# Kernel optimization log

Measured on AMD Instinct MI355X. Metric: run time of the kernel, lower is better.

Reference implementation:

```python
import jax, jax.numpy as jnp
import numpy as np

N, E, B = 50000, 400000, 128
F_IN, EDIM, EMB, H = 64, 8, 64, 4
HC = EMB * H  # 256
L = 3          # gnn_layers
DN = 256       # dense_neurons
NEG_SLOPE = 0.2
EPS = 1e-5


def setup_inputs():
    key = jax.random.key(0)
    ks = jax.random.split(key, 32)
    s = 0.05
    d = {}
    d["x"] = jax.random.normal(ks[0], (N, F_IN), jnp.float32)
    d["edge_index"] = jax.random.randint(ks[1], (2, E), 0, N, jnp.int32)
    d["edge_attr"] = jax.random.normal(ks[2], (E, EDIM), jnp.float32)
    d["mol_formal_charge"] = jax.random.normal(ks[3], (B,), jnp.float32)
    d["mol_nrot"] = jax.random.normal(ks[4], (B,), jnp.float32)
    d["batch_index"] = jnp.sort(jax.random.randint(ks[5], (N,), 0, B, jnp.int32))
    # GATv2 params, stacked over L layers (in_dim == EMB == F_IN for all layers)
    d["gat_Wl"] = jax.random.normal(ks[6], (L, F_IN, HC), jnp.float32) * s
    d["gat_Wr"] = jax.random.normal(ks[7], (L, F_IN, HC), jnp.float32) * s
    d["gat_We"] = jax.random.normal(ks[8], (L, EDIM, HC), jnp.float32) * s
    d["gat_att"] = jax.random.normal(ks[9], (L, H, EMB), jnp.float32) * s
    d["gat_b"] = jnp.zeros((L, HC), jnp.float32)
    d["tr_W"] = jax.random.normal(ks[10], (L, HC, EMB), jnp.float32) * s
    d["tr_b"] = jnp.zeros((L, EMB), jnp.float32)
    d["bn_g"] = jnp.ones((L, EMB), jnp.float32)
    d["bn_b"] = jnp.zeros((L, EMB), jnp.float32)
    d["gate_W"] = jax.random.normal(ks[11], (EMB, 1), jnp.float32) * s
    d["gate_b"] = jnp.zeros((1,), jnp.float32)
    d["lin1_W"] = jax.random.normal(ks[12], (EMB + 2, DN), jnp.float32) * s
    d["lin1_b"] = jnp.zeros((DN,), jnp.float32)
    d["fc1_W"] = jax.random.normal(ks[13], (DN, DN // 2), jnp.float32) * s
    d["fc1_b"] = jnp.zeros((DN // 2,), jnp.float32)
    d["fc2_W"] = jax.random.normal(ks[14], (DN // 2, DN // 4), jnp.float32) * s
    d["fc2_b"] = jnp.zeros((DN // 4,), jnp.float32)
    d["out_W"] = jax.random.normal(ks[15], (DN // 4, 1), jnp.float32) * s
    d["out_b"] = jnp.zeros((1,), jnp.float32)
    return d


def _seg_softmax(logits, seg, num):
    # numerically stable per-segment softmax over leading axis
    mx = jax.ops.segment_max(logits, seg, num_segments=num)
    ex = jnp.exp(logits - mx[seg])
    den = jax.ops.segment_sum(ex, seg, num_segments=num)
    return ex / den[seg]


def reference(x, edge_index, edge_attr, mol_formal_charge, mol_nrot, batch_index,
              gat_Wl, gat_Wr, gat_We, gat_att, gat_b, tr_W, tr_b, bn_g, bn_b,
              gate_W, gate_b, lin1_W, lin1_b, fc1_W, fc1_b, fc2_W, fc2_b,
              out_W, out_b):
    src, dst = edge_index[0], edge_index[1]  # messages flow src -> dst
    h = x
    for l in range(L):
        xl = (h @ gat_Wl[l]).reshape(N, H, EMB)
        xr = (h @ gat_Wr[l]).reshape(N, H, EMB)
        ea = (edge_attr @ gat_We[l]).reshape(E, H, EMB)
        xls = xl[src]                                   # [E,H,C]
        m = jax.nn.leaky_relu(xls + xr[dst] + ea, NEG_SLOPE)
        logit = jnp.einsum('ehc,hc->eh', m, gat_att[l])  # [E,H]
        alpha = _seg_softmax(logit, dst, N)              # [E,H]
        agg = jax.ops.segment_sum(alpha[:, :, None] * xls, dst, num_segments=N)
        h = agg.reshape(N, HC) + gat_b[l]
        h = jax.nn.relu(h @ tr_W[l] + tr_b[l])
        # BatchNorm1d (training-mode batch stats, biased var)
        mu = h.mean(0)
        var = h.var(0)
        h = (h - mu) / jnp.sqrt(var + EPS) * bn_g[l] + bn_b[l]
    # AttentionalAggregation pooling
    gate = h @ gate_W + gate_b                           # [N,1]
    w = _seg_softmax(gate, batch_index, B)
    pooled = jax.ops.segment_sum(w * h, batch_index, num_segments=B)  # [B,EMB]
    z = jnp.concatenate([pooled, mol_formal_charge[:, None], mol_nrot[:, None]], axis=1)
    z = jax.nn.relu(z @ lin1_W + lin1_b)
    z = jax.nn.relu(z @ fc1_W + fc1_b)
    z = jax.nn.relu(z @ fc2_W + fc2_b)
    return z @ out_W + out_b                             # [B,1]
```

## Files before the change

kernel.cpp:

```cpp
#include <hip/hip_runtime.h>

#define NN 50000
#define NE 400000
#define NB 128
#define NINF (-__builtin_inff())

__device__ __forceinline__ float dpp_add16(float x) {
    int v = __float_as_int(x);
    x += __int_as_float(__builtin_amdgcn_update_dpp(0, v, 0xB1, 0xF, 0xF, true));
    v = __float_as_int(x);
    x += __int_as_float(__builtin_amdgcn_update_dpp(0, v, 0x4E, 0xF, 0xF, true));
    v = __float_as_int(x);
    x += __int_as_float(__builtin_amdgcn_update_dpp(0, v, 0x141, 0xF, 0xF, true));
    v = __float_as_int(x);
    x += __int_as_float(__builtin_amdgcn_update_dpp(0, v, 0x140, 0xF, 0xF, true));
    return x;
}

__global__ __launch_bounds__(256) void k_hist(const int* __restrict__ dstv, int* __restrict__ deg) {
    int e = blockIdx.x * 256 + threadIdx.x;
    if (e < NE) atomicAdd(&deg[dstv[e]], 1);
}

__global__ __launch_bounds__(256) void k_scan1(const int* __restrict__ deg, int* __restrict__ bsum,
                                               int* __restrict__ cnt) {
    __shared__ int ws[4];
    const int tid = threadIdx.x, lane = tid & 63, w = tid >> 6;
    const int i = blockIdx.x * 256 + tid;
    if (i < NN) cnt[i] = 0;
    int v = (i < NN) ? deg[i] : 0;
    #pragma unroll
    for (int off = 32; off; off >>= 1) v += __shfl_xor(v, off);
    if (lane == 0) ws[w] = v;
    __syncthreads();
    if (tid == 0) bsum[blockIdx.x] = ws[0] + ws[1] + ws[2] + ws[3];
}

__global__ __launch_bounds__(256) void k_scan2(const int* __restrict__ bsum, int* __restrict__ boff, int nblk,
                                               float* __restrict__ stats) {
    __shared__ int ws[4];
    const int tid = threadIdx.x, lane = tid & 63, w = tid >> 6;
    for (int i = tid; i < 2304; i += 256) stats[i] = 0.f;
    int v = (tid < nblk) ? bsum[tid] : 0;
    int incl = v;
    #pragma unroll
    for (int off = 1; off < 64; off <<= 1) {
        int t = __shfl_up(incl, off);
        if (lane >= off) incl += t;
    }
    if (lane == 63) ws[w] = incl;
    __syncthreads();
    int add = 0;
    for (int k = 0; k < w; ++k) add += ws[k];
    if (tid < nblk) boff[tid] = add + incl - v;
}

__global__ __launch_bounds__(256) void k_scan3(const int* __restrict__ deg, const int* __restrict__ boff,
                                               int* __restrict__ rowptr) {
    __shared__ int ws[4];
    const int tid = threadIdx.x, lane = tid & 63, w = tid >> 6;
    const int i = blockIdx.x * 256 + tid;
    int v = (i < NN) ? deg[i] : 0;
    int incl = v;
    #pragma unroll
    for (int off = 1; off < 64; off <<= 1) {
        int t = __shfl_up(incl, off);
        if (lane >= off) incl += t;
    }
    if (lane == 63) ws[w] = incl;
    __syncthreads();
    int add = boff[blockIdx.x];
    for (int k = 0; k < w; ++k) add += ws[k];
    if (i < NN) rowptr[i + 1] = add + incl;
    if (i == 0) rowptr[0] = 0;
}

__global__ __launch_bounds__(256) void k_scatter(const int* __restrict__ dstv, const int* __restrict__ srcv,
                                                 const float* __restrict__ eattr, const int* __restrict__ rowptr,
                                                 int* __restrict__ cnt, int* __restrict__ eid,
                                                 int* __restrict__ src_perm, float4* __restrict__ ea_perm,
                                                 int use_perm) {
    int e = blockIdx.x * 256 + threadIdx.x;
    if (e < NE) {
        int d = dstv[e];
        int pos = rowptr[d] + atomicAdd(&cnt[d], 1);
        eid[pos] = e;
        if (use_perm) {
            src_perm[pos] = srcv[e];
            ea_perm[(size_t)pos * 2] = ((const float4*)eattr)[e * 2];
            ea_perm[(size_t)pos * 2 + 1] = ((const float4*)eattr)[e * 2 + 1];
        }
    }
}

__global__ __launch_bounds__(256) void k_bnfin(float* __restrict__ st, const float* __restrict__ g,
                                               const float* __restrict__ b, const float* __restrict__ Wln,
                                               const float* __restrict__ Wrn) {
    __shared__ float sh_s[64];
    const int tid = threadIdx.x;
    if (tid < 64) {
        const float mu = st[tid] * (1.0f / (float)NN);
        const float var = st[64 + tid] * (1.0f / (float)NN) - mu * mu;
        const float rstd = rsqrtf(var + 1e-5f);
        const float sc = g[tid] * rstd;
        const float sh = fmaf(-mu, sc, b[tid]);
        st[128 + tid] = sc;
        st[192 + tid] = sh;
        sh_s[tid] = sh;
    }
    __syncthreads();
    float al = 0.f, ar = 0.f;
    for (int k = 0; k < 64; ++k) {
        al = fmaf(sh_s[k], Wln[k * 256 + tid], al);
        ar = fmaf(sh_s[k], Wrn[k * 256 + tid], ar);
    }
    st[256 + tid] = al;
    st[512 + tid] = ar;
}

__global__ __launch_bounds__(256, 4) void k_gemm64(const float* __restrict__ A, const float* __restrict__ Wl,
                                                   const float* __restrict__ Wr, float* __restrict__ Cl,
                                                   float* __restrict__ Cr, const float* __restrict__ stats) {
    __shared__ float At[16 * 132];
    __shared__ float Ws[16 * 128];
    const int tid = threadIdx.x;
    const int mat = blockIdx.y >> 1, ch = blockIdx.y & 1;
    const float* W = mat ? Wr : Wl;
    float* C = mat ? Cr : Cl;
    const int r0b = blockIdx.x * 128;
    const int cg = tid & 15;
    const int rg = tid >> 4;

    float acc[8][8];
    if (stats) {
        const float* shW = stats + 256 + mat * 256 + ch * 128;
        const float4 i0 = *(const float4*)(shW + cg * 4);
        const float4 i1 = *(const float4*)(shW + 64 + cg * 4);
        #pragma unroll
        for (int rr = 0; rr < 8; ++rr) {
            acc[rr][0] = i0.x; acc[rr][1] = i0.y; acc[rr][2] = i0.z; acc[rr][3] = i0.w;
            acc[rr][4] = i1.x; acc[rr][5] = i1.y; acc[rr][6] = i1.z; acc[rr][7] = i1.w;
        }
    } else {
        #pragma unroll
        for (int rr = 0; rr < 8; ++rr)
            #pragma unroll
            for (int j = 0; j < 8; ++j) acc[rr][j] = 0.f;
    }

    for (int kc = 0; kc < 4; ++kc) {
        if (kc) __syncthreads();
        for (int i = tid; i < 512; i += 256) {
            const int k = i >> 5, c4 = i & 31;
            float4 v = ((const float4*)W)[(kc * 16 + k) * 64 + ch * 32 + c4];
            if (stats) {
                const float s = stats[128 + kc * 16 + k];
                v.x *= s; v.y *= s; v.z *= s; v.w *= s;
            }
            ((float4*)Ws)[i] = v;
        }
        for (int i = tid; i < 512; i += 256) {
            const int r = i >> 2, c4 = i & 3;
            const int rgl = (r0b + r < NN) ? (r0b + r) : (NN - 1);
            const float4 v = ((const float4*)A)[rgl * 16 + kc * 4 + c4];
            At[(c4 * 4 + 0) * 132 + r] = v.x;
            At[(c4 * 4 + 1) * 132 + r] = v.y;
            At[(c4 * 4 + 2) * 132 + r] = v.z;
            At[(c4 * 4 + 3) * 132 + r] = v.w;
        }
        __syncthreads();
        #pragma unroll 4
        for (int k = 0; k < 16; ++k) {
            const float4 a0 = *(const float4*)(At + k * 132 + rg * 8);
            const float4 a1 = *(const float4*)(At + k * 132 + rg * 8 + 4);
            const float4 w0 = *(const float4*)(Ws + k * 128 + cg * 4);
            const float4 w1 = *(const float4*)(Ws + k * 128 + 64 + cg * 4);
            const float ar[8] = {a0.x, a0.y, a0.z, a0.w, a1.x, a1.y, a1.z, a1.w};
            #pragma unroll
            for (int rr = 0; rr < 8; ++rr) {
                acc[rr][0] = fmaf(ar[rr], w0.x, acc[rr][0]);
                acc[rr][1] = fmaf(ar[rr], w0.y, acc[rr][1]);
                acc[rr][2] = fmaf(ar[rr], w0.z, acc[rr][2]);
                acc[rr][3] = fmaf(ar[rr], w0.w, acc[rr][3]);
                acc[rr][4] = fmaf(ar[rr], w1.x, acc[rr][4]);
                acc[rr][5] = fmaf(ar[rr], w1.y, acc[rr][5]);
                acc[rr][6] = fmaf(ar[rr], w1.z, acc[rr][6]);
                acc[rr][7] = fmaf(ar[rr], w1.w, acc[rr][7]);
            }
        }
    }
    #pragma unroll
    for (int rr = 0; rr < 8; ++rr) {
        const int r = r0b + rg * 8 + rr;
        if (r < NN) {
            float* cp = C + (size_t)r * 256 + ch * 128 + cg * 4;
            *(float4*)cp = make_float4(acc[rr][0], acc[rr][1], acc[rr][2], acc[rr][3]);
            *(float4*)(cp + 64) = make_float4(acc[rr][4], acc[rr][5], acc[rr][6], acc[rr][7]);
        }
    }
}

template <bool PERM>
__global__ __launch_bounds__(256, 4) void k_agg(const float* __restrict__ xl, float* __restrict__ xragg,
                                                const float* __restrict__ att, const float* __restrict__ gatb,
                                                const int* __restrict__ rowptr, const int* __restrict__ eid,
                                                const int* __restrict__ srcv, const float* __restrict__ eattr,
                                                const int* __restrict__ src_perm, const float4* __restrict__ ea_perm,
                                                const float* __restrict__ We) {
    const int lane = threadIdx.x & 63;
    const float4 we0 = ((const float4*)(We + 0 * 256))[lane];
    const float4 we1 = ((const float4*)(We + 1 * 256))[lane];
    const float4 we2 = ((const float4*)(We + 2 * 256))[lane];
    const float4 we3 = ((const float4*)(We + 3 * 256))[lane];
    const float4 we4 = ((const float4*)(We + 4 * 256))[lane];
    const float4 we5 = ((const float4*)(We + 5 * 256))[lane];
    const float4 we6 = ((const float4*)(We + 6 * 256))[lane];
    const float4 we7 = ((const float4*)(We + 7 * 256))[lane];
    const float4 attf = ((const float4*)att)[lane];
    const float4 gbf = ((const float4*)gatb)[lane];
    const int nw = gridDim.x * (blockDim.x >> 6);
    const int wid = blockIdx.x * (blockDim.x >> 6) + (threadIdx.x >> 6);

#define LOADE(X, idx)                                                          \
    {                                                                          \
        int s_;                                                                \
        const float4* eap_;                                                    \
        if (PERM) {                                                            \
            s_ = src_perm[idx];                                                \
            eap_ = ea_perm + (size_t)(idx) * 2;                                \
        } else {                                                               \
            const int e_ = eid[idx];                                           \
            s_ = srcv[e_];                                                     \
            eap_ = (const float4*)(eattr + (size_t)e_ * 8);                    \
        }                                                                      \
        X##x = ((const float4*)(xl + (size_t)s_ * 256))[lane];                 \
        X##a = eap_[0];                                                        \
        X##b = eap_[1];                                                        \
    }

#define PROC(X)                                                                \
    {                                                                          \
        float v0 = fmaf(X##a.x, we0.x, xr.x), v1 = fmaf(X##a.x, we0.y, xr.y);  \
        float v2 = fmaf(X##a.x, we0.z, xr.z), v3 = fmaf(X##a.x, we0.w, xr.w);  \
        v0 = fmaf(X##a.y, we1.x, v0); v1 = fmaf(X##a.y, we1.y, v1);            \
        v2 = fmaf(X##a.y, we1.z, v2); v3 = fmaf(X##a.y, we1.w, v3);            \
        v0 = fmaf(X##a.z, we2.x, v0); v1 = fmaf(X##a.z, we2.y, v1);            \
        v2 = fmaf(X##a.z, we2.z, v2); v3 = fmaf(X##a.z, we2.w, v3);            \
        v0 = fmaf(X##a.w, we3.x, v0); v1 = fmaf(X##a.w, we3.y, v1);            \
        v2 = fmaf(X##a.w, we3.z, v2); v3 = fmaf(X##a.w, we3.w, v3);            \
        v0 = fmaf(X##b.x, we4.x, v0); v1 = fmaf(X##b.x, we4.y, v1);            \
        v2 = fmaf(X##b.x, we4.z, v2); v3 = fmaf(X##b.x, we4.w, v3);            \
        v0 = fmaf(X##b.y, we5.x, v0); v1 = fmaf(X##b.y, we5.y, v1);            \
        v2 = fmaf(X##b.y, we5.z, v2); v3 = fmaf(X##b.y, we5.w, v3);            \
        v0 = fmaf(X##b.z, we6.x, v0); v1 = fmaf(X##b.z, we6.y, v1);            \
        v2 = fmaf(X##b.z, we6.z, v2); v3 = fmaf(X##b.z, we6.w, v3);            \
        v0 = fmaf(X##b.w, we7.x, v0); v1 = fmaf(X##b.w, we7.y, v1);            \
        v2 = fmaf(X##b.w, we7.z, v2); v3 = fmaf(X##b.w, we7.w, v3);            \
        v0 += X##x.x; v1 += X##x.y; v2 += X##x.z; v3 += X##x.w;                \
        v0 = fmaxf(v0, 0.2f * v0); v1 = fmaxf(v1, 0.2f * v1);                  \
        v2 = fmaxf(v2, 0.2f * v2); v3 = fmaxf(v3, 0.2f * v3);                  \
        float part = v0 * attf.x;                                              \
        part = fmaf(v1, attf.y, part);                                         \
        part = fmaf(v2, attf.z, part);                                         \
        part = fmaf(v3, attf.w, part);                                         \
        part = dpp_add16(part);                                                \
        const float p = __expf(part);                                          \
        den += p;                                                              \
        c0 = fmaf(p, X##x.x, c0);                                              \
        c1 = fmaf(p, X##x.y, c1);                                              \
        c2 = fmaf(p, X##x.z, c2);                                              \
        c3 = fmaf(p, X##x.w, c3);                                              \
    }

    for (int n = wid; n < NN; n += nw) {
        const int e0 = rowptr[n], e1 = rowptr[n + 1];
        const float4 xr = ((const float4*)(xragg + (size_t)n * 256))[lane];
        float den = 0.f, c0 = 0.f, c1 = 0.f, c2 = 0.f, c3 = 0.f;
        float4 Ax, Aa, Ab, Bx, Ba, Bb, Cx, Ca, Cb;
        const int cnt = e1 - e0;
        if (cnt > 0) {
            LOADE(A, e0);
            if (cnt > 1) LOADE(B, e0 + 1);
            if (cnt > 2) LOADE(C, e0 + 2);
            int i = e0;
            for (; i + 5 < e1; i += 3) {
                PROC(A);
                LOADE(A, i + 3);
                PROC(B);
                LOADE(B, i + 4);
                PROC(C);
                LOADE(C, i + 5);
            }
            const int m = e1 - i;
            PROC(A);
            if (m >= 2) PROC(B);
            if (m >= 3) PROC(C);
            if (m >= 4) { LOADE(A, i + 3); PROC(A); }
            if (m == 5) { LOADE(B, i + 4); PROC(B); }
        }
        float4 o;
        if (cnt > 0) {
            const float inv = 1.0f / den;
            o.x = fmaf(c0, inv, gbf.x);
            o.y = fmaf(c1, inv, gbf.y);
            o.z = fmaf(c2, inv, gbf.z);
            o.w = fmaf(c3, inv, gbf.w);
        } else {
            o = gbf;
        }
        ((float4*)(xragg + (size_t)n * 256))[lane] = o;
    }
#undef LOADE
#undef PROC
}

__global__ __launch_bounds__(256, 4) void k_tr(const float* __restrict__ A, const float* __restrict__ W,
                                               const float* __restrict__ bias, float* __restrict__ Hout,
                                               float* __restrict__ stats) {
    __shared__ float At[16 * 260];
    __shared__ float Ws[16 * 64];
    __shared__ float red[128];
    const int tid = threadIdx.x;
    const int cg = tid & 7;
    const int rg = tid >> 3;
    const int r0b = blockIdx.x * 256;

    float acc[8][8];
    #pragma unroll
    for (int rr = 0; rr < 8; ++rr)
        #pragma unroll
        for (int j = 0; j < 8; ++j)
            acc[rr][j] = bias[cg * 8 + j];

    for (int kc = 0; kc < 16; ++kc) {
        if (kc) __syncthreads();
        if (tid < 256) ((float4*)Ws)[tid] = ((const float4*)(W + kc * 1024))[tid];
        for (int i = tid; i < 1024; i += 256) {
            const int r = i >> 2, c4 = i & 3;
            const int rgl = (r0b + r < NN) ? (r0b + r) : (NN - 1);
            const float4 v = ((const float4*)A)[(size_t)rgl * 64 + kc * 4 + c4];
            At[(c4 * 4 + 0) * 260 + r] = v.x;
            At[(c4 * 4 + 1) * 260 + r] = v.y;
            At[(c4 * 4 + 2) * 260 + r] = v.z;
            At[(c4 * 4 + 3) * 260 + r] = v.w;
        }
        __syncthreads();
        #pragma unroll 4
        for (int k = 0; k < 16; ++k) {
            const float4 a0 = *(const float4*)(At + k * 260 + rg * 8);
            const float4 a1 = *(const float4*)(At + k * 260 + rg * 8 + 4);
            const float4 w0 = *(const float4*)(Ws + k * 64 + cg * 8);
            const float4 w1 = *(const float4*)(Ws + k * 64 + cg * 8 + 4);
            const float ar[8] = {a0.x, a0.y, a0.z, a0.w, a1.x, a1.y, a1.z, a1.w};
            #pragma unroll
            for (int rr = 0; rr < 8; ++rr) {
                acc[rr][0] = fmaf(ar[rr], w0.x, acc[rr][0]);
                acc[rr][1] = fmaf(ar[rr], w0.y, acc[rr][1]);
                acc[rr][2] = fmaf(ar[rr], w0.z, acc[rr][2]);
                acc[rr][3] = fmaf(ar[rr], w0.w, acc[rr][3]);
                acc[rr][4] = fmaf(ar[rr], w1.x, acc[rr][4]);
                acc[rr][5] = fmaf(ar[rr], w1.y, acc[rr][5]);
                acc[rr][6] = fmaf(ar[rr], w1.z, acc[rr][6]);
                acc[rr][7] = fmaf(ar[rr], w1.w, acc[rr][7]);
            }
        }
    }
    float lsum[8], lsq[8];
    #pragma unroll
    for (int j = 0; j < 8; ++j) { lsum[j] = 0.f; lsq[j] = 0.f; }
    #pragma unroll
    for (int rr = 0; rr < 8; ++rr) {
        const int r = r0b + rg * 8 + rr;
        if (r < NN) {
            float v[8];
            #pragma unroll
            for (int j = 0; j < 8; ++j) {
                v[j] = fmaxf(acc[rr][j], 0.f);
                lsum[j] += v[j];
                lsq[j] = fmaf(v[j], v[j], lsq[j]);
            }
            float* hp = Hout + (size_t)r * 64;
            *(float4*)(hp + cg * 8) = make_float4(v[0], v[1], v[2], v[3]);
            *(float4*)(hp + cg * 8 + 4) = make_float4(v[4], v[5], v[6], v[7]);
        }
    }
    __syncthreads();
    if (tid < 128) red[tid] = 0.f;
    __syncthreads();
    #pragma unroll
    for (int j = 0; j < 8; ++j) {
        atomicAdd(&red[cg * 8 + j], lsum[j]);
        atomicAdd(&red[64 + cg * 8 + j], lsq[j]);
    }
    __syncthreads();
    if (tid < 64) {
        atomicAdd(&stats[tid], red[tid]);
        atomicAdd(&stats[64 + tid], red[64 + tid]);
    }
}

__global__ __launch_bounds__(256) void k_poolhead(const float* __restrict__ h, const float* __restrict__ gw,
                                                  const int* __restrict__ bidx, const float* __restrict__ stats,
                                                  const float* __restrict__ bg, const float* __restrict__ bb,
                                                  const float* __restrict__ fc, const float* __restrict__ nrot,
                                                  const float* __restrict__ W1, const float* __restrict__ b1,
                                                  const float* __restrict__ W2, const float* __restrict__ b2,
                                                  const float* __restrict__ W3, const float* __restrict__ b3,
                                                  const float* __restrict__ W4, const float* __restrict__ b4,
                                                  float* __restrict__ out) {
    __shared__ float gate_s[1024];
    __shared__ float red[4];
    __shared__ float pp[4][64];
    __shared__ float scb[64], shb[64];
    __shared__ float z[66], a1[256], a2[128], a3[64];
    const int b = blockIdx.x, tid = threadIdx.x, lane = tid & 63, w = tid >> 6;
    if (tid < 64) {
        const float mu = stats[tid] * (1.0f / (float)NN);
        const float var = stats[64 + tid] * (1.0f / (float)NN) - mu * mu;
        const float rstd = rsqrtf(var + 1e-5f);
        const float sc = bg[tid] * rstd;
        scb[tid] = sc;
        shb[tid] = fmaf(-mu, sc, bb[tid]);
    }
    int lo = 0, hi = NN;
    while (lo < hi) { int mid = (lo + hi) >> 1; if (bidx[mid] < b) lo = mid + 1; else hi = mid; }
    const int s0 = lo;
    lo = 0; hi = NN;
    while (lo < hi) { int mid = (lo + hi) >> 1; if (bidx[mid] < b + 1) lo = mid + 1; else hi = mid; }
    const int s1 = lo;
    const int seg = s1 - s0;
    __syncthreads();

    const float gwv = gw[lane] * scb[lane];
    for (int i = s0 + w; i < s1; i += 4) {
        float p = h[(size_t)i * 64 + lane] * gwv;
        #pragma unroll
        for (int off = 32; off; off >>= 1) p += __shfl_xor(p, off);
        if (lane == 0) gate_s[i - s0] = p;
    }
    __syncthreads();
    float v = NINF;
    for (int i = tid; i < seg; i += 256) v = fmaxf(v, gate_s[i]);
    #pragma unroll
    for (int off = 32; off; off >>= 1) v = fmaxf(v, __shfl_xor(v, off));
    if (lane == 0) red[w] = v;
    __syncthreads();
    const float mx = fmaxf(fmaxf(red[0], red[1]), fmaxf(red[2], red[3]));
    __syncthreads();
    float d = 0.f;
    for (int i = tid; i < seg; i += 256) {
        const float ex = __expf(gate_s[i] - mx);
        gate_s[i] = ex;
        d += ex;
    }
    #pragma unroll
    for (int off = 32; off; off >>= 1) d += __shfl_xor(d, off);
    if (lane == 0) red[w] = d;
    __syncthreads();
    const float den = red[0] + red[1] + red[2] + red[3];
    const int c = tid & 63, ro = tid >> 6;
    float acc = 0.f;
    for (int i = s0 + ro; i < s1; i += 4) acc = fmaf(gate_s[i - s0], h[(size_t)i * 64 + c], acc);
    pp[ro][c] = acc;
    __syncthreads();
    if (tid < 64) {
        const float raw = (pp[0][tid] + pp[1][tid] + pp[2][tid] + pp[3][tid]) / den;
        z[tid] = (seg > 0) ? fmaf(raw, scb[tid], shb[tid]) : shb[tid];
    }
    if (tid == 64) z[64] = fc[b];
    if (tid == 65) z[65] = nrot[b];
    __syncthreads();
    float s = b1[tid];
    for (int k = 0; k < 66; ++k) s = fmaf(z[k], W1[k * 256 + tid], s);
    a1[tid] = fmaxf(s, 0.f);
    __syncthreads();
    if (tid < 128) {
        float s2 = b2[tid];
        for (int k = 0; k < 256; ++k) s2 = fmaf(a1[k], W2[k * 128 + tid], s2);
        a2[tid] = fmaxf(s2, 0.f);
    }
    __syncthreads();
    if (tid < 64) {
        float s3 = b3[tid];
        for (int k = 0; k < 128; ++k) s3 = fmaf(a2[k], W3[k * 64 + tid], s3);
        a3[tid] = fmaxf(s3, 0.f);
    }
    __syncthreads();
    if (tid < 64) {
        float p = a3[tid] * W4[tid];
        #pragma unroll
        for (int off = 32; off; off >>= 1) p += __shfl_xor(p, off);
        if (tid == 0) out[b] = p + b4[0];
    }
}

extern "C" void kernel_launch(void* const* d_in, const int* in_sizes, int n_in,
                              void* d_out, int out_size, void* d_ws, size_t ws_size,
                              hipStream_t stream) {
    const float* x     = (const float*)d_in[0];
    const int*   ei    = (const int*)d_in[1];
    const float* eattr = (const float*)d_in[2];
    const float* fcv   = (const float*)d_in[3];
    const float* nrot  = (const float*)d_in[4];
    const int*   bidx  = (const int*)d_in[5];
    const float* Wl    = (const float*)d_in[6];
    const float* Wr    = (const float*)d_in[7];
    const float* We    = (const float*)d_in[8];
    const float* att   = (const float*)d_in[9];
    const float* gatb  = (const float*)d_in[10];
    const float* trW   = (const float*)d_in[11];
    const float* trb   = (const float*)d_in[12];
    const float* bng   = (const float*)d_in[13];
    const float* bnb   = (const float*)d_in[14];
    const float* gateW = (const float*)d_in[15];
    const float* W1    = (const float*)d_in[17];
    const float* b1    = (const float*)d_in[18];
    const float* W2    = (const float*)d_in[19];
    const float* b2    = (const float*)d_in[20];
    const float* W3    = (const float*)d_in[21];
    const float* b3    = (const float*)d_in[22];
    const float* W4    = (const float*)d_in[23];
    const float* b4    = (const float*)d_in[24];
    float* out = (float*)d_out;

    const int* srcv = ei;
    const int* dstv = ei + NE;

    char* w = (char*)d_ws;
    float*  xl       = (float*)(w);
    float*  xragg    = (float*)(w + 51200000);
    float*  hbuf     = (float*)(w + 102400000);
    int*    deg      = (int*)  (w + 102400000);
    int*    cnt      = (int*)  (w + 102600000);
    int*    eid      = (int*)  (w + 115200000);
    int*    rowptr   = (int*)  (w + 116800000);
    float*  stats    = (float*)(w + 117000064);
    int*    bsum     = (int*)  (w + 117010176);
    int*    boff     = (int*)  (w + 117012224);
    int*    src_perm = (int*)  (w + 117042048);
    float4* ea_perm  = (float4*)(w + 118642048);
    const bool use_perm = (ws_size >= (size_t)131442048);
    const int NBLK = (NN + 255) / 256;

    hipMemsetAsync(deg, 0, 200000, stream);
    k_hist<<<(NE + 255) / 256, 256, 0, stream>>>(dstv, deg);
    k_scan1<<<NBLK, 256, 0, stream>>>(deg, bsum, cnt);
    k_scan2<<<1, 256, 0, stream>>>(bsum, boff, NBLK, stats);
    k_scan3<<<NBLK, 256, 0, stream>>>(deg, boff, rowptr);
    k_scatter<<<(NE + 255) / 256, 256, 0, stream>>>(dstv, srcv, eattr, rowptr, cnt, eid,
                                                    src_perm, ea_perm, use_perm ? 1 : 0);

    const float* hin = x;
    for (int l = 0; l < 3; ++l) {
        const float* st = (l == 0) ? nullptr : (stats + (l - 1) * 768);
        dim3 gg((NN + 127) / 128, 4);
        k_gemm64<<<gg, 256, 0, stream>>>(hin, Wl + l * 16384, Wr + l * 16384, xl, xragg, st);
        if (use_perm)
            k_agg<true><<<2048, 256, 0, stream>>>(xl, xragg, att + l * 256, gatb + l * 256, rowptr,
                                                  eid, srcv, eattr, src_perm, ea_perm, We + l * 2048);
        else
            k_agg<false><<<2048, 256, 0, stream>>>(xl, xragg, att + l * 256, gatb + l * 256, rowptr,
                                                   eid, srcv, eattr, src_perm, ea_perm, We + l * 2048);
        k_tr<<<(NN + 255) / 256, 256, 0, stream>>>(xragg, trW + l * 16384, trb + l * 64, hbuf, stats + l * 768);
        if (l < 2)
            k_bnfin<<<1, 256, 0, stream>>>(stats + l * 768, bng + l * 64, bnb + l * 64,
                                           Wl + (l + 1) * 16384, Wr + (l + 1) * 16384);
        hin = hbuf;
    }
    k_poolhead<<<NB, 256, 0, stream>>>(hbuf, gateW, bidx, stats + 2 * 768, bng + 128, bnb + 128,
                                       fcv, nrot, W1, b1, W2, b2, W3, b3, W4, b4, out);
}
```

Measured before the change: 726.0 us.

## Fuse BatchNorm finalize into transform kernel and double GEMM K-tile depth

Result: no change. 717.9 us (-1.1%).

```diff
diff --git a/kernel.cpp b/kernel.cpp
--- a/kernel.cpp
+++ b/kernel.cpp
@@ -40,7 +40,7 @@
                                                float* __restrict__ stats) {
     __shared__ int ws[4];
     const int tid = threadIdx.x, lane = tid & 63, w = tid >> 6;
-    for (int i = tid; i < 2304; i += 256) stats[i] = 0.f;
+    for (int i = tid; i < 2308; i += 256) stats[i] = 0.f;
     int v = (tid < nblk) ? bsum[tid] : 0;
     int incl = v;
     #pragma unroll
@@ -93,36 +93,11 @@
     }
 }
 
-__global__ __launch_bounds__(256) void k_bnfin(float* __restrict__ st, const float* __restrict__ g,
-                                               const float* __restrict__ b, const float* __restrict__ Wln,
-                                               const float* __restrict__ Wrn) {
-    __shared__ float sh_s[64];
-    const int tid = threadIdx.x;
-    if (tid < 64) {
-        const float mu = st[tid] * (1.0f / (float)NN);
-        const float var = st[64 + tid] * (1.0f / (float)NN) - mu * mu;
-        const float rstd = rsqrtf(var + 1e-5f);
-        const float sc = g[tid] * rstd;
-        const float sh = fmaf(-mu, sc, b[tid]);
-        st[128 + tid] = sc;
-        st[192 + tid] = sh;
-        sh_s[tid] = sh;
-    }
-    __syncthreads();
-    float al = 0.f, ar = 0.f;
-    for (int k = 0; k < 64; ++k) {
-        al = fmaf(sh_s[k], Wln[k * 256 + tid], al);
-        ar = fmaf(sh_s[k], Wrn[k * 256 + tid], ar);
-    }
-    st[256 + tid] = al;
-    st[512 + tid] = ar;
-}
-
 __global__ __launch_bounds__(256, 4) void k_gemm64(const float* __restrict__ A, const float* __restrict__ Wl,
                                                    const float* __restrict__ Wr, float* __restrict__ Cl,
                                                    float* __restrict__ Cr, const float* __restrict__ stats) {
-    __shared__ float At[16 * 132];
-    __shared__ float Ws[16 * 128];
+    __shared__ float At[32 * 132];
+    __shared__ float Ws[32 * 128];
     const int tid = threadIdx.x;
     const int mat = blockIdx.y >> 1, ch = blockIdx.y & 1;
     const float* W = mat ? Wr : Wl;
@@ -148,21 +123,21 @@
             for (int j = 0; j < 8; ++j) acc[rr][j] = 0.f;
     }
 
-    for (int kc = 0; kc < 4; ++kc) {
+    for (int kc = 0; kc < 2; ++kc) {
         if (kc) __syncthreads();
-        for (int i = tid; i < 512; i += 256) {
+        for (int i = tid; i < 1024; i += 256) {
             const int k = i >> 5, c4 = i & 31;
-            float4 v = ((const float4*)W)[(kc * 16 + k) * 64 + ch * 32 + c4];
+            float4 v = ((const float4*)W)[(kc * 32 + k) * 64 + ch * 32 + c4];
             if (stats) {
-                const float s = stats[128 + kc * 16 + k];
+                const float s = stats[128 + kc * 32 + k];
                 v.x *= s; v.y *= s; v.z *= s; v.w *= s;
             }
             ((float4*)Ws)[i] = v;
         }
-        for (int i = tid; i < 512; i += 256) {
-            const int r = i >> 2, c4 = i & 3;
+        for (int i = tid; i < 1024; i += 256) {
+            const int r = i >> 3, c4 = i & 7;
             const int rgl = (r0b + r < NN) ? (r0b + r) : (NN - 1);
-            const float4 v = ((const float4*)A)[rgl * 16 + kc * 4 + c4];
+            const float4 v = ((const float4*)A)[rgl * 16 + kc * 8 + c4];
             At[(c4 * 4 + 0) * 132 + r] = v.x;
             At[(c4 * 4 + 1) * 132 + r] = v.y;
             At[(c4 * 4 + 2) * 132 + r] = v.z;
@@ -170,7 +145,7 @@
         }
         __syncthreads();
         #pragma unroll 4
-        for (int k = 0; k < 16; ++k) {
+        for (int k = 0; k < 32; ++k) {
             const float4 a0 = *(const float4*)(At + k * 132 + rg * 8);
             const float4 a1 = *(const float4*)(At + k * 132 + rg * 8 + 4);
             const float4 w0 = *(const float4*)(Ws + k * 128 + cg * 4);
@@ -316,10 +291,14 @@
 
 __global__ __launch_bounds__(256, 4) void k_tr(const float* __restrict__ A, const float* __restrict__ W,
                                                const float* __restrict__ bias, float* __restrict__ Hout,
-                                               float* __restrict__ stats) {
-    __shared__ float At[16 * 260];
-    __shared__ float Ws[16 * 64];
+                                               float* __restrict__ stats, const float* __restrict__ g,
+                                               const float* __restrict__ b, const float* __restrict__ Wln,
+                                               const float* __restrict__ Wrn, int* __restrict__ done,
+                                               int do_fin) {
+    __shared__ float At[32 * 260];
+    __shared__ float Ws[32 * 64];
     __shared__ float red[128];
+    __shared__ int isLast;
     const int tid = threadIdx.x;
     const int cg = tid & 7;
     const int rg = tid >> 3;
@@ -332,13 +311,14 @@
         for (int j = 0; j < 8; ++j)
             acc[rr][j] = bias[cg * 8 + j];
 
-    for (int kc = 0; kc < 16; ++kc) {
+    for (int kc = 0; kc < 8; ++kc) {
         if (kc) __syncthreads();
-        if (tid < 256) ((float4*)Ws)[tid] = ((const float4*)(W + kc * 1024))[tid];
-        for (int i = tid; i < 1024; i += 256) {
-            const int r = i >> 2, c4 = i & 3;
+        for (int i = tid; i < 512; i += 256)
+            ((float4*)Ws)[i] = ((const float4*)(W + kc * 2048))[i];
+        for (int i = tid; i < 2048; i += 256) {
+            const int r = i >> 3, c4 = i & 7;
             const int rgl = (r0b + r < NN) ? (r0b + r) : (NN - 1);
-            const float4 v = ((const float4*)A)[(size_t)rgl * 64 + kc * 4 + c4];
+            const float4 v = ((const float4*)A)[(size_t)rgl * 64 + kc * 8 + c4];
             At[(c4 * 4 + 0) * 260 + r] = v.x;
             At[(c4 * 4 + 1) * 260 + r] = v.y;
             At[(c4 * 4 + 2) * 260 + r] = v.z;
@@ -346,7 +326,7 @@
         }
         __syncthreads();
         #pragma unroll 4
-        for (int k = 0; k < 16; ++k) {
+        for (int k = 0; k < 32; ++k) {
             const float4 a0 = *(const float4*)(At + k * 260 + rg * 8);
             const float4 a1 = *(const float4*)(At + k * 260 + rg * 8 + 4);
             const float4 w0 = *(const float4*)(Ws + k * 64 + cg * 8);
@@ -397,6 +377,34 @@
         atomicAdd(&stats[tid], red[tid]);
         atomicAdd(&stats[64 + tid], red[64 + tid]);
     }
+    if (!do_fin) return;
+    __threadfence();
+    if (tid == 0) {
+        const int t = atomicAdd(done, 1);
+        isLast = (t == (int)gridDim.x - 1);
+    }
+    __syncthreads();
+    if (!isLast) return;
+    if (tid < 64) {
+        const float sum = atomicAdd(&stats[tid], 0.f);
+        const float sq  = atomicAdd(&stats[64 + tid], 0.f);
+        const float mu = sum * (1.0f / (float)NN);
+        const float var = sq * (1.0f / (float)NN) - mu * mu;
+        const float rstd = rsqrtf(var + 1e-5f);
+        const float sc = g[tid] * rstd;
+        const float sh = fmaf(-mu, sc, b[tid]);
+        stats[128 + tid] = sc;
+        stats[192 + tid] = sh;
+        red[tid] = sh;
+    }
+    __syncthreads();
+    float al = 0.f, ar = 0.f;
+    for (int k = 0; k < 64; ++k) {
+        al = fmaf(red[k], Wln[k * 256 + tid], al);
+        ar = fmaf(red[k], Wrn[k * 256 + tid], ar);
+    }
+    stats[256 + tid] = al;
+    stats[512 + tid] = ar;
 }
 
 __global__ __launch_bounds__(256) void k_poolhead(const float* __restrict__ h, const float* __restrict__ gw,
@@ -535,6 +543,7 @@
     int*    eid      = (int*)  (w + 115200000);
     int*    rowptr   = (int*)  (w + 116800000);
     float*  stats    = (float*)(w + 117000064);
+    int*    done     = (int*)  (w + 117000064 + 2304 * 4);
     int*    bsum     = (int*)  (w + 117010176);
     int*    boff     = (int*)  (w + 117012224);
     int*    src_perm = (int*)  (w + 117042048);
@@ -561,10 +570,11 @@
         else
             k_agg<false><<<2048, 256, 0, stream>>>(xl, xragg, att + l * 256, gatb + l * 256, rowptr,
                                                    eid, srcv, eattr, src_perm, ea_perm, We + l * 2048);
-        k_tr<<<(NN + 255) / 256, 256, 0, stream>>>(xragg, trW + l * 16384, trb + l * 64, hbuf, stats + l * 768);
-        if (l < 2)
-            k_bnfin<<<1, 256, 0, stream>>>(stats + l * 768, bng + l * 64, bnb + l * 64,
-                                           Wl + (l + 1) * 16384, Wr + (l + 1) * 16384);
+        const float* Wln = (l < 2) ? (Wl + (l + 1) * 16384) : Wl;
+        const float* Wrn = (l < 2) ? (Wr + (l + 1) * 16384) : Wr;
+        k_tr<<<(NN + 255) / 256, 256, 0, stream>>>(xragg, trW + l * 16384, trb + l * 64, hbuf,
+                                                   stats + l * 768, bng + l * 64, bnb + l * 64,
+                                                   Wln, Wrn, done + l, (l < 2) ? 1 : 0);
         hin = hbuf;
     }
     k_poolhead<<<NB, 256, 0, stream>>>(hbuf, gateW, bidx, stats + 2 * 768, bng + 128, bnb + 128,
```
